# Kernel tuning notes

Hardware: AMD Instinct MI355X
Metric: run time of the kernel (lower is better)

## Reference

```python
import jax, jax.numpy as jnp
import numpy as np

N = 50000      # nodes
E = 1600000    # edges (avg degree 32)
F_IN = 128
HID = 256
C = 40


def setup_inputs() -> dict:
    key = jax.random.key(0)
    ks = jax.random.split(key, 12)
    x = jax.random.normal(ks[0], (N, F_IN), jnp.float32)
    edge_index = jax.random.randint(ks[1], (2, E), 0, N, dtype=jnp.int32)

    def glorot(k, fan_in, fan_out):
        s = jnp.sqrt(2.0 / (fan_in + fan_out)).astype(jnp.float32)
        return jax.random.normal(k, (fan_in, fan_out), jnp.float32) * s

    return {
        "x": x,
        "edge_index": edge_index,
        "W1": glorot(ks[2], F_IN, HID), "b1": jnp.zeros((HID,), jnp.float32),
        "W2": glorot(ks[3], HID, HID),  "b2": jnp.zeros((HID,), jnp.float32),
        "W3": glorot(ks[4], HID, HID),  "b3": jnp.zeros((HID,), jnp.float32),
        "W4": glorot(ks[5], HID, C),    "b4": jnp.zeros((C,), jnp.float32),
    }


def _gcn_conv(x, W, b, src, dst, norm_e, self_norm):
    # PyG GCNConv: h = X W; out_j = sum_i norm_ij * h_i  (+ self-loop term) + b
    h = x @ W                                   # [N, F_out]
    msg = h[src] * norm_e[:, None]              # [E, F_out] gather + scale
    agg = jax.ops.segment_sum(msg, dst, num_segments=N)
    agg = agg + h * self_norm[:, None]          # self-loop contribution
    return agg + b


def reference(x, edge_index, W1, b1, W2, b2, W3, b3, W4, b4):
    src, dst = edge_index[0], edge_index[1]
    # degree on A + I (self-loops added), computed over destination nodes
    deg = jax.ops.segment_sum(jnp.ones((E,), x.dtype), dst, num_segments=N) + 1.0
    inv_sqrt = jax.lax.rsqrt(deg)               # [N]
    norm_e = inv_sqrt[src] * inv_sqrt[dst]      # [E] symmetric norm per edge
    self_norm = inv_sqrt * inv_sqrt             # [N] self-loop norm = 1/deg

    h = jax.nn.relu(_gcn_conv(x, W1, b1, src, dst, norm_e, self_norm))
    h = jax.nn.relu(_gcn_conv(h, W2, b2, src, dst, norm_e, self_norm))
    h = jax.nn.relu(_gcn_conv(h, W3, b3, src, dst, norm_e, self_norm))
    h = _gcn_conv(h, W4, b4, src, dst, norm_e, self_norm)
    return jax.nn.log_softmax(h, axis=1)
```

## Files before the change

### kernel.cpp

```cpp
#include <hip/hip_runtime.h>
#include <hip/hip_fp16.h>
#include <math.h>


typedef _Float16 f16x8 __attribute__((ext_vector_type(8)));
typedef float f32x4 __attribute__((ext_vector_type(4)));

#define CAP 80

#define AS1 __attribute__((address_space(1)))
#define AS3 __attribute__((address_space(3)))

__device__ __forceinline__ void dma16(const unsigned short* g,
                                      const unsigned short* ldsBase) {
    __builtin_amdgcn_global_load_lds((const AS1 void*)(size_t)g,
                                     (AS3 void*)(unsigned)(size_t)ldsBase,
                                     16, 0, 0);
}

__device__ __forceinline__ __half2 u2h2(unsigned u) {
    union { unsigned u; __half2 h; } v; v.u = u; return v.h;
}
__device__ __forceinline__ unsigned h22u(__half2 h) {
    union { unsigned u; __half2 h; } v; v.h = h; return v.u;
}
__device__ __forceinline__ float hlo(unsigned u) {
    return __half2float(__ushort_as_half((unsigned short)(u & 0xFFFFu)));
}
__device__ __forceinline__ float hhi(unsigned u) {
    return __half2float(__ushort_as_half((unsigned short)(u >> 16)));
}

__global__ __launch_bounds__(256) void countprep_kernel(
        const int* __restrict__ src, const int* __restrict__ dst,
        int* __restrict__ cnt, int* __restrict__ rank, int E, int nEdgeBlocks,
        const float* __restrict__ x, unsigned short* __restrict__ xb, int nx4,
        const float* __restrict__ W1, const float* __restrict__ W2,
        const float* __restrict__ W3, const float* __restrict__ W4,
        unsigned short* __restrict__ Wt1, unsigned short* __restrict__ Wt2,
        unsigned short* __restrict__ Wt3, unsigned short* __restrict__ Wt4) {
    int b = blockIdx.x;
    if (b < nEdgeBlocks) {
        int e = b * 256 + threadIdx.x;
        if (e < E) rank[e] = atomicAdd(&cnt[dst[e]], 1);
        return;
    }
    int i = (b - nEdgeBlocks) * 256 + threadIdx.x;
    if (i < nx4) {
        float4 v = reinterpret_cast<const float4*>(x)[i];
        ushort4 o;
        o.x = __half_as_ushort(__float2half_rn(v.x));
        o.y = __half_as_ushort(__float2half_rn(v.y));
        o.z = __half_as_ushort(__float2half_rn(v.z));
        o.w = __half_as_ushort(__float2half_rn(v.w));
        reinterpret_cast<ushort4*>(xb)[i] = o;
        return;
    }
    int j = i - nx4;
    if (j < 32768) {
        int k = j >> 8, n = j & 255;
        Wt1[n * 128 + k] = __half_as_ushort(__float2half_rn(W1[j]));
    } else if (j < 98304) {
        int t = j - 32768; int k = t >> 8, n = t & 255;
        Wt2[n * 256 + k] = __half_as_ushort(__float2half_rn(W2[t]));
    } else if (j < 163840) {
        int t = j - 98304; int k = t >> 8, n = t & 255;
        Wt3[n * 256 + k] = __half_as_ushort(__float2half_rn(W3[t]));
    } else if (j < 174080) {
        int t = j - 163840; int k = t / 40, n = t - k * 40;
        Wt4[n * 256 + k] = __half_as_ushort(__float2half_rn(W4[t]));
    }
}

__global__ __launch_bounds__(256) void rsq_kernel(const int* __restrict__ cnt,
                                                  float* __restrict__ rsq, int N) {
    int n = blockIdx.x * 256 + threadIdx.x;
    if (n < N) rsq[n] = rsqrtf((float)cnt[n] + 1.0f);
}

__global__ __launch_bounds__(256) void scatter_kernel(const int* __restrict__ src,
                                                      const int* __restrict__ dst,
                                                      const int* __restrict__ rank,
                                                      const float* __restrict__ rsq,
                                                      unsigned* __restrict__ epk, int E) {
    int e = blockIdx.x * 256 + threadIdx.x;
    if (e < E) {
        int d = dst[e];
        int s = src[e];
        int r = rank[e]; if (r >= CAP) r = CAP - 1;
        float w = rsq[s] * rsq[d];
        epk[(size_t)d * CAP + r] = (unsigned)s |
                   ((unsigned)__half_as_ushort(__float2half_rn(w)) << 16);
    }
}

template <int H2, bool BIAS, bool RELU>
__global__ __launch_bounds__(256) void agg_f16_kernel(
        const unsigned* __restrict__ G,
        const int* __restrict__ cnt,
        const unsigned* __restrict__ epk,
        const float* __restrict__ rsq,
        const float* __restrict__ bias,
        unsigned* __restrict__ out, int N) {
    constexpr int ROWU = 64 * H2;
    constexpr int UNR = 8;
    int lane = threadIdx.x & 63;
    int node = blockIdx.x * 4 + (threadIdx.x >> 6);
    if (node >= N) return;
    const unsigned* base = G + lane * H2;
    const unsigned* ep = epk + (size_t)node * CAP;
    int deg = cnt[node];

    __half2 acc[H2];
    #pragma unroll
    for (int i = 0; i < H2; i++) acc[i] = u2h2(0u);

    int e = 0;
    for (; e + UNR - 1 < deg; e += UNR) {
        unsigned p[UNR];
        int s[UNR];
        #pragma unroll
        for (int j = 0; j < UNR; j++) { p[j] = ep[e + j]; s[j] = p[j] & 0xFFFFu; }
        unsigned g[UNR][H2];
        #pragma unroll
        for (int j = 0; j < UNR; j++)
            #pragma unroll
            for (int i = 0; i < H2; i++)
                g[j][i] = base[(size_t)s[j] * ROWU + i];
        #pragma unroll
        for (int j = 0; j < UNR; j++) {
            __half2 w2 = __half2half2(__ushort_as_half((unsigned short)(p[j] >> 16)));
            #pragma unroll
            for (int i = 0; i < H2; i++)
                acc[i] = __hfma2(w2, u2h2(g[j][i]), acc[i]);
        }
    }
    for (; e < deg; e++) {
        unsigned p0 = ep[e];
        int s0 = p0 & 0xFFFFu;
        __half2 w2 = __half2half2(__ushort_as_half((unsigned short)(p0 >> 16)));
        #pragma unroll
        for (int i = 0; i < H2; i++)
            acc[i] = __hfma2(w2, u2h2(base[(size_t)s0 * ROWU + i]), acc[i]);
    }

    float sn = rsq[node];
    sn *= sn;
    #pragma unroll
    for (int i = 0; i < H2; i++) {
        unsigned sv = base[(size_t)node * ROWU + i];
        float2 f = __half22float2(acc[i]);
        f.x = fmaf(sn, hlo(sv), f.x);
        f.y = fmaf(sn, hhi(sv), f.y);
        if (BIAS) {
            float2 b = reinterpret_cast<const float2*>(bias)[lane * H2 + i];
            f.x += b.x; f.y += b.y;
        }
        if (RELU) { f.x = fmaxf(f.x, 0.f); f.y = fmaxf(f.y, 0.f); }
        out[(size_t)node * ROWU + lane * H2 + i] = h22u(__floats2half2_rn(f.x, f.y));
    }
}

__global__ __launch_bounds__(256) void agg40_softmax_kernel(
        const unsigned* __restrict__ G,
        const int* __restrict__ cnt,
        const unsigned* __restrict__ epk,
        const float* __restrict__ rsq,
        const float* __restrict__ bias,
        float* __restrict__ out, int N) {
    int lane = threadIdx.x & 63;
    int node = blockIdx.x * 4 + (threadIdx.x >> 6);
    if (node >= N) return;
    bool act = lane < 20;
    int cl = act ? lane : 0;
    const unsigned* ep = epk + (size_t)node * CAP;
    int deg = cnt[node];
    __half2 acch = u2h2(0u);
    int e = 0;
    for (; e + 3 < deg; e += 4) {
        unsigned p[4];
        int s[4];
        #pragma unroll
        for (int j = 0; j < 4; j++) { p[j] = ep[e + j]; s[j] = p[j] & 0xFFFFu; }
        unsigned g[4];
        #pragma unroll
        for (int j = 0; j < 4; j++) g[j] = G[(size_t)s[j] * 20 + cl];
        #pragma unroll
        for (int j = 0; j < 4; j++) {
            __half2 w = __half2half2(__ushort_as_half((unsigned short)(p[j] >> 16)));
            acch = __hfma2(w, u2h2(g[j]), acch);
        }
    }
    for (; e < deg; e++) {
        unsigned p0 = ep[e];
        int s0 = p0 & 0xFFFFu;
        __half2 w0 = __half2half2(__ushort_as_half((unsigned short)(p0 >> 16)));
        acch = __hfma2(w0, u2h2(G[(size_t)s0 * 20 + cl]), acch);
    }
    float lo = 0.f, hi = 0.f;
    if (act) {
        float sn = rsq[node];
        sn *= sn;
        unsigned sv = G[(size_t)node * 20 + lane];
        float2 f = __half22float2(acch);
        lo = fmaf(sn, hlo(sv), f.x) + bias[2 * lane];
        hi = fmaf(sn, hhi(sv), f.y) + bias[2 * lane + 1];
    }
    float m = act ? fmaxf(lo, hi) : -INFINITY;
    #pragma unroll
    for (int o = 32; o >= 1; o >>= 1) m = fmaxf(m, __shfl_xor(m, o, 64));
    float s = act ? (expf(lo - m) + expf(hi - m)) : 0.f;
    #pragma unroll
    for (int o = 32; o >= 1; o >>= 1) s += __shfl_xor(s, o, 64);
    float ls = logf(s);
    if (act) {
        float2 o2;
        o2.x = lo - m - ls;
        o2.y = hi - m - ls;
        *reinterpret_cast<float2*>(out + (size_t)node * 40 + 2 * lane) = o2;
    }
}

template <bool BIAS, bool RELU>
__global__ __launch_bounds__(256) void gemm_f16(
        const unsigned short* __restrict__ A,
        const unsigned short* __restrict__ Bt,
        const float* __restrict__ bias,
        unsigned short* __restrict__ Cout,
        int M, int K, int Nc) {
    __shared__ __align__(16) unsigned short As[128 * 64];
    __shared__ __align__(16) unsigned short Bs[128 * 64];
    int tid = threadIdx.x;
    int lane = tid & 63;
    int wid = tid >> 6;
    int rowBase = blockIdx.y * 128;
    int colBase = blockIdx.x * 128;
    int waveM = (wid & 1) * 64;
    int waveN = (wid >> 1) * 64;

    f32x4 acc[4][4] = {};
    int lrow = lane & 15;
    int kgrp = (lane >> 4) * 8;

    for (int k0 = 0; k0 < K; k0 += 64) {
        #pragma unroll
        for (int c = 0; c < 4; c++) {
            int base16 = c * 256 + wid * 64;
            int slot = base16 + lane;
            int row = slot >> 3;
            int kp = (slot & 7) * 8;
            int ksw = kp ^ ((row & 7) * 8);
            int gr = rowBase + row; if (gr >= M) gr = M - 1;
            dma16(A + (size_t)gr * K + k0 + ksw, &As[base16 * 8]);
            int gc = colBase + row; if (gc >= Nc) gc = Nc - 1;
            dma16(Bt + (size_t)gc * K + k0 + ksw, &Bs[base16 * 8]);
        }
        __syncthreads();
        #pragma unroll
        for (int kk = 0; kk < 64; kk += 32) {
            f16x8 af[4], bfr[4];
            #pragma unroll
            for (int t = 0; t < 4; t++) {
                int ra = waveM + t * 16 + lrow;
                af[t] = *reinterpret_cast<const f16x8*>(
                    &As[ra * 64 + ((kk + kgrp) ^ ((ra & 7) * 8))]);
                int rb = waveN + t * 16 + lrow;
                bfr[t] = *reinterpret_cast<const f16x8*>(
                    &Bs[rb * 64 + ((kk + kgrp) ^ ((rb & 7) * 8))]);
            }
            #pragma unroll
            for (int mt = 0; mt < 4; mt++)
                #pragma unroll
                for (int nt = 0; nt < 4; nt++)
                    acc[mt][nt] = __builtin_amdgcn_mfma_f32_16x16x32_f16(
                        af[mt], bfr[nt], acc[mt][nt], 0, 0, 0);
        }
        __syncthreads();
    }

    #pragma unroll
    for (int mt = 0; mt < 4; mt++) {
        #pragma unroll
        for (int r = 0; r < 4; r++) {
            int row = rowBase + waveM + mt * 16 + (lane >> 4) * 4 + r;
            if (row >= M) continue;
            #pragma unroll
            for (int nt = 0; nt < 4; nt++) {
                int col = colBase + waveN + nt * 16 + (lane & 15);
                if (col >= Nc) continue;
                float v = acc[mt][nt][r];
                if (BIAS) v += bias[col];
                if (RELU) v = fmaxf(v, 0.f);
                Cout[(size_t)row * Nc + col] = __half_as_ushort(__float2half_rn(v));
            }
        }
    }
}


extern "C" void kernel_launch(void* const* d_in, const int* in_sizes, int n_in,
                              void* d_out, int out_size, void* d_ws, size_t ws_size,
                              hipStream_t stream) {
    const float* x  = (const float*)d_in[0];
    const int*   ei = (const int*)d_in[1];
    const float* W1 = (const float*)d_in[2];
    const float* b1 = (const float*)d_in[3];
    const float* W2 = (const float*)d_in[4];
    const float* b2 = (const float*)d_in[5];
    const float* W3 = (const float*)d_in[6];
    const float* b3 = (const float*)d_in[7];
    const float* W4 = (const float*)d_in[8];
    const float* b4 = (const float*)d_in[9];

    const int FIN = 128, HID = 256, C = 40;
    const int N = in_sizes[0] / FIN;
    const int E = in_sizes[1] / 2;
    const int* src = ei;
    const int* dst = ei + E;

    char* w = (char*)d_ws;
    auto alloc = [&](size_t bytes) {
        char* p = w;
        w += (bytes + 255) & ~(size_t)255;
        return p;
    };
    int*   cnt    = (int*)alloc((size_t)N * 4);
    float* rsq    = (float*)alloc((size_t)N * 4);
    unsigned* epk = (unsigned*)alloc((size_t)N * CAP * 4);
    unsigned short* aggx = (unsigned short*)alloc((size_t)N * FIN * 2);
    unsigned short* bufA = (unsigned short*)alloc((size_t)N * HID * 2);
    unsigned short* bufB = (unsigned short*)alloc((size_t)N * HID * 2);
    unsigned short* Wt1 = (unsigned short*)alloc((size_t)FIN * HID * 2);
    unsigned short* Wt2 = (unsigned short*)alloc((size_t)HID * HID * 2);
    unsigned short* Wt3 = (unsigned short*)alloc((size_t)HID * HID * 2);
    unsigned short* Wt4 = (unsigned short*)alloc((size_t)HID * C * 2);
    int* rank = (int*)aggx;
    unsigned short* xb = bufB;

    hipMemsetAsync(cnt, 0, (size_t)N * 4, stream);

    int nx4 = N * FIN / 4;
    int nEdgeBlocks = (E + 255) / 256;
    int prepBlocks = (nx4 + 174080 + 255) / 256;
    countprep_kernel<<<nEdgeBlocks + prepBlocks, 256, 0, stream>>>(
        src, dst, cnt, rank, E, nEdgeBlocks,
        x, xb, nx4, W1, W2, W3, W4, Wt1, Wt2, Wt3, Wt4);
    rsq_kernel<<<(N + 255) / 256, 256, 0, stream>>>(cnt, rsq, N);
    scatter_kernel<<<nEdgeBlocks, 256, 0, stream>>>(src, dst, rank, rsq, epk, E);

    int grp = (N + 3) / 4;
    dim3 gHID((HID + 127) / 128, (N + 127) / 128);
    dim3 gC((C + 127) / 128, (N + 127) / 128);

    agg_f16_kernel<1, false, false>
        <<<grp, 256, 0, stream>>>((const unsigned*)xb, cnt, epk, rsq, nullptr,
                                  (unsigned*)aggx, N);
    gemm_f16<true, true><<<gHID, 256, 0, stream>>>(aggx, Wt1, b1, bufA, N, FIN, HID);
    gemm_f16<false, false><<<gHID, 256, 0, stream>>>(bufA, Wt2, nullptr, bufB,
                                                     N, HID, HID);
    agg_f16_kernel<2, true, true>
        <<<grp, 256, 0, stream>>>((const unsigned*)bufB, cnt, epk, rsq, b2,
                                  (unsigned*)bufA, N);
    gemm_f16<false, false><<<gHID, 256, 0, stream>>>(bufA, Wt3, nullptr, bufB,
                                                     N, HID, HID);
    agg_f16_kernel<2, true, true>
        <<<grp, 256, 0, stream>>>((const unsigned*)bufB, cnt, epk, rsq, b3,
                                  (unsigned*)bufA, N);
    gemm_f16<false, false><<<gC, 256, 0, stream>>>(bufA, Wt4, nullptr, bufB,
                                                   N, HID, C);
    agg40_softmax_kernel<<<grp, 256, 0, stream>>>((const unsigned*)bufB, cnt, epk,
                                                  rsq, b4, (float*)d_out, N);
}
```

Before: 585.4 us.

## Fold symmetric norm into node-side scaling and shrink edge lists to 16-bit indices

The separate scatter kernel goes away: the count kernel now writes 16-bit source indices straight into the capped per-node adjacency slots. Per-edge weights are no longer stored. The D^-1/2 factors are moved onto node rows instead: hidden features are kept pre-scaled by rsq, so later aggregations become plain half-precision adds, and the output scaling, bias and ReLU are applied per node in the epilogue. The GEMM K-tile is also raised to 128. This cuts edge-list bandwidth in half and drops one kernel launch, at the cost of extra rsq gathers in the first layer and different fp16 rounding behaviour.

```diff
diff --git a/kernel.cpp b/kernel.cpp
--- a/kernel.cpp
+++ b/kernel.cpp
@@ -31,9 +31,10 @@
     return __half2float(__ushort_as_half((unsigned short)(u >> 16)));
 }
 
-__global__ __launch_bounds__(256) void countprep_kernel(
+__global__ __launch_bounds__(256) void build_prep_kernel(
         const int* __restrict__ src, const int* __restrict__ dst,
-        int* __restrict__ cnt, int* __restrict__ rank, int E, int nEdgeBlocks,
+        int* __restrict__ cnt, unsigned short* __restrict__ epk,
+        int E, int nEdgeBlocks,
         const float* __restrict__ x, unsigned short* __restrict__ xb, int nx4,
         const float* __restrict__ W1, const float* __restrict__ W2,
         const float* __restrict__ W3, const float* __restrict__ W4,
@@ -42,7 +43,12 @@
     int b = blockIdx.x;
     if (b < nEdgeBlocks) {
         int e = b * 256 + threadIdx.x;
-        if (e < E) rank[e] = atomicAdd(&cnt[dst[e]], 1);
+        if (e < E) {
+            int d = dst[e];
+            int s = src[e];
+            int r = atomicAdd(&cnt[d], 1);
+            if (r < CAP) epk[(size_t)d * CAP + r] = (unsigned short)s;
+        }
         return;
     }
     int i = (b - nEdgeBlocks) * 256 + threadIdx.x;
@@ -78,93 +84,101 @@
     if (n < N) rsq[n] = rsqrtf((float)cnt[n] + 1.0f);
 }
 
-__global__ __launch_bounds__(256) void scatter_kernel(const int* __restrict__ src,
-                                                      const int* __restrict__ dst,
-                                                      const int* __restrict__ rank,
-                                                      const float* __restrict__ rsq,
-                                                      unsigned* __restrict__ epk, int E) {
-    int e = blockIdx.x * 256 + threadIdx.x;
-    if (e < E) {
-        int d = dst[e];
-        int s = src[e];
-        int r = rank[e]; if (r >= CAP) r = CAP - 1;
-        float w = rsq[s] * rsq[d];
-        epk[(size_t)d * CAP + r] = (unsigned)s |
-                   ((unsigned)__half_as_ushort(__float2half_rn(w)) << 16);
-    }
-}
-
-template <int H2, bool BIAS, bool RELU>
-__global__ __launch_bounds__(256) void agg_f16_kernel(
+template <int H2, bool WSRC, bool BIAS, bool RELU>
+__global__ __launch_bounds__(256) void agg_sum_kernel(
         const unsigned* __restrict__ G,
         const int* __restrict__ cnt,
-        const unsigned* __restrict__ epk,
+        const unsigned short* __restrict__ epk,
         const float* __restrict__ rsq,
         const float* __restrict__ bias,
         unsigned* __restrict__ out, int N) {
     constexpr int ROWU = 64 * H2;
-    constexpr int UNR = 8;
     int lane = threadIdx.x & 63;
     int node = blockIdx.x * 4 + (threadIdx.x >> 6);
     if (node >= N) return;
     const unsigned* base = G + lane * H2;
-    const unsigned* ep = epk + (size_t)node * CAP;
-    int deg = cnt[node];
+    const unsigned short* ep = epk + (size_t)node * CAP;
+    int deg = cnt[node]; if (deg > CAP) deg = CAP;
 
     __half2 acc[H2];
     #pragma unroll
     for (int i = 0; i < H2; i++) acc[i] = u2h2(0u);
 
     int e = 0;
-    for (; e + UNR - 1 < deg; e += UNR) {
-        unsigned p[UNR];
-        int s[UNR];
-        #pragma unroll
-        for (int j = 0; j < UNR; j++) { p[j] = ep[e + j]; s[j] = p[j] & 0xFFFFu; }
-        unsigned g[UNR][H2];
-        #pragma unroll
-        for (int j = 0; j < UNR; j++)
+    for (; e + 7 < deg; e += 8) {
+        uint4 pv = *reinterpret_cast<const uint4*>(ep + e);
+        int s[8];
+        s[0] = pv.x & 0xFFFFu; s[1] = pv.x >> 16;
+        s[2] = pv.y & 0xFFFFu; s[3] = pv.y >> 16;
+        s[4] = pv.z & 0xFFFFu; s[5] = pv.z >> 16;
+        s[6] = pv.w & 0xFFFFu; s[7] = pv.w >> 16;
+        float ws[8];
+        if (WSRC) {
+            #pragma unroll
+            for (int j = 0; j < 8; j++) ws[j] = rsq[s[j]];
+        }
+        unsigned g[8][H2];
+        #pragma unroll
+        for (int j = 0; j < 8; j++)
             #pragma unroll
             for (int i = 0; i < H2; i++)
                 g[j][i] = base[(size_t)s[j] * ROWU + i];
         #pragma unroll
-        for (int j = 0; j < UNR; j++) {
-            __half2 w2 = __half2half2(__ushort_as_half((unsigned short)(p[j] >> 16)));
+        for (int j = 0; j < 8; j++) {
+            if (WSRC) {
+                __half2 w2 = __half2half2(__float2half_rn(ws[j]));
+                #pragma unroll
+                for (int i = 0; i < H2; i++)
+                    acc[i] = __hfma2(w2, u2h2(g[j][i]), acc[i]);
+            } else {
+                #pragma unroll
+                for (int i = 0; i < H2; i++)
+                    acc[i] = __hadd2(acc[i], u2h2(g[j][i]));
+            }
+        }
+    }
+    for (; e < deg; e++) {
+        int s0 = ep[e];
+        if (WSRC) {
+            __half2 w2 = __half2half2(__float2half_rn(rsq[s0]));
             #pragma unroll
             for (int i = 0; i < H2; i++)
-                acc[i] = __hfma2(w2, u2h2(g[j][i]), acc[i]);
-        }
-    }
-    for (; e < deg; e++) {
-        unsigned p0 = ep[e];
-        int s0 = p0 & 0xFFFFu;
-        __half2 w2 = __half2half2(__ushort_as_half((unsigned short)(p0 >> 16)));
-        #pragma unroll
-        for (int i = 0; i < H2; i++)
-            acc[i] = __hfma2(w2, u2h2(base[(size_t)s0 * ROWU + i]), acc[i]);
-    }
-
-    float sn = rsq[node];
-    sn *= sn;
+                acc[i] = __hfma2(w2, u2h2(base[(size_t)s0 * ROWU + i]), acc[i]);
+        } else {
+            #pragma unroll
+            for (int i = 0; i < H2; i++)
+                acc[i] = __hadd2(acc[i], u2h2(base[(size_t)s0 * ROWU + i]));
+        }
+    }
+
+    float r = rsq[node];
+    float sw = WSRC ? r : 1.0f;
     #pragma unroll
     for (int i = 0; i < H2; i++) {
+        float2 f = __half22float2(acc[i]);
         unsigned sv = base[(size_t)node * ROWU + i];
-        float2 f = __half22float2(acc[i]);
-        f.x = fmaf(sn, hlo(sv), f.x);
-        f.y = fmaf(sn, hhi(sv), f.y);
-        if (BIAS) {
-            float2 b = reinterpret_cast<const float2*>(bias)[lane * H2 + i];
-            f.x += b.x; f.y += b.y;
-        }
-        if (RELU) { f.x = fmaxf(f.x, 0.f); f.y = fmaxf(f.y, 0.f); }
-        out[(size_t)node * ROWU + lane * H2 + i] = h22u(__floats2half2_rn(f.x, f.y));
+        f.x = fmaf(sw, hlo(sv), f.x);
+        f.y = fmaf(sw, hhi(sv), f.y);
+        float ox, oy;
+        if (WSRC) {
+            ox = r * f.x; oy = r * f.y;
+        } else {
+            float r2 = r * r;
+            ox = r2 * f.x; oy = r2 * f.y;
+            if (BIAS) {
+                float2 bv = reinterpret_cast<const float2*>(bias)[lane * H2 + i];
+                ox = fmaf(r, bv.x, ox); oy = fmaf(r, bv.y, oy);
+            }
+            if (RELU) { ox = fmaxf(ox, 0.f); oy = fmaxf(oy, 0.f); }
+        }
+        out[(size_t)node * ROWU + lane * H2 + i] = h22u(__floats2half2_rn(ox, oy));
     }
 }
 
 __global__ __launch_bounds__(256) void agg40_softmax_kernel(
         const unsigned* __restrict__ G,
         const int* __restrict__ cnt,
-        const unsigned* __restrict__ epk,
+        const unsigned short* __restrict__ epk,
         const float* __restrict__ rsq,
         const float* __restrict__ bias,
         float* __restrict__ out, int N) {
@@ -173,38 +187,35 @@
     if (node >= N) return;
     bool act = lane < 20;
     int cl = act ? lane : 0;
-    const unsigned* ep = epk + (size_t)node * CAP;
-    int deg = cnt[node];
+    const unsigned short* ep = epk + (size_t)node * CAP;
+    int deg = cnt[node]; if (deg > CAP) deg = CAP;
     __half2 acch = u2h2(0u);
     int e = 0;
-    for (; e + 3 < deg; e += 4) {
-        unsigned p[4];
-        int s[4];
-        #pragma unroll
-        for (int j = 0; j < 4; j++) { p[j] = ep[e + j]; s[j] = p[j] & 0xFFFFu; }
-        unsigned g[4];
-        #pragma unroll
-        for (int j = 0; j < 4; j++) g[j] = G[(size_t)s[j] * 20 + cl];
-        #pragma unroll
-        for (int j = 0; j < 4; j++) {
-            __half2 w = __half2half2(__ushort_as_half((unsigned short)(p[j] >> 16)));
-            acch = __hfma2(w, u2h2(g[j]), acch);
-        }
+    for (; e + 7 < deg; e += 8) {
+        uint4 pv = *reinterpret_cast<const uint4*>(ep + e);
+        int s[8];
+        s[0] = pv.x & 0xFFFFu; s[1] = pv.x >> 16;
+        s[2] = pv.y & 0xFFFFu; s[3] = pv.y >> 16;
+        s[4] = pv.z & 0xFFFFu; s[5] = pv.z >> 16;
+        s[6] = pv.w & 0xFFFFu; s[7] = pv.w >> 16;
+        unsigned g[8];
+        #pragma unroll
+        for (int j = 0; j < 8; j++) g[j] = G[(size_t)s[j] * 20 + cl];
+        #pragma unroll
+        for (int j = 0; j < 8; j++) acch = __hadd2(acch, u2h2(g[j]));
     }
     for (; e < deg; e++) {
-        unsigned p0 = ep[e];
-        int s0 = p0 & 0xFFFFu;
-        __half2 w0 = __half2half2(__ushort_as_half((unsigned short)(p0 >> 16)));
-        acch = __hfma2(w0, u2h2(G[(size_t)s0 * 20 + cl]), acch);
+        int s0 = ep[e];
+        acch = __hadd2(acch, u2h2(G[(size_t)s0 * 20 + cl]));
     }
     float lo = 0.f, hi = 0.f;
     if (act) {
-        float sn = rsq[node];
-        sn *= sn;
+        float r = rsq[node];
         unsigned sv = G[(size_t)node * 20 + lane];
         float2 f = __half22float2(acch);
-        lo = fmaf(sn, hlo(sv), f.x) + bias[2 * lane];
-        hi = fmaf(sn, hhi(sv), f.y) + bias[2 * lane + 1];
+        f.x += hlo(sv); f.y += hhi(sv);
+        lo = fmaf(r, f.x, bias[2 * lane]);
+        hi = fmaf(r, f.y, bias[2 * lane + 1]);
     }
     float m = act ? fmaxf(lo, hi) : -INFINITY;
     #pragma unroll
@@ -221,15 +232,18 @@
     }
 }
 
-template <bool BIAS, bool RELU>
+template <int BK, bool BIAS, bool RELU, bool SCALE>
 __global__ __launch_bounds__(256) void gemm_f16(
         const unsigned short* __restrict__ A,
         const unsigned short* __restrict__ Bt,
         const float* __restrict__ bias,
+        const float* __restrict__ rsqRow,
         unsigned short* __restrict__ Cout,
         int M, int K, int Nc) {
-    __shared__ __align__(16) unsigned short As[128 * 64];
-    __shared__ __align__(16) unsigned short Bs[128 * 64];
+    constexpr int SPR = BK / 8;
+    constexpr int NSTG = (128 * SPR) / 256;
+    __shared__ __align__(16) unsigned short As[128 * BK];
+    __shared__ __align__(16) unsigned short Bs[128 * BK];
     int tid = threadIdx.x;
     int lane = tid & 63;
     int wid = tid >> 6;
@@ -242,14 +256,14 @@
     int lrow = lane & 15;
     int kgrp = (lane >> 4) * 8;
 
-    for (int k0 = 0; k0 < K; k0 += 64) {
-        #pragma unroll
-        for (int c = 0; c < 4; c++) {
+    for (int k0 = 0; k0 < K; k0 += BK) {
+        #pragma unroll
+        for (int c = 0; c < NSTG; c++) {
             int base16 = c * 256 + wid * 64;
             int slot = base16 + lane;
-            int row = slot >> 3;
-            int kp = (slot & 7) * 8;
-            int ksw = kp ^ ((row & 7) * 8);
+            int row = slot / SPR;
+            int kp = (slot % SPR) * 8;
+            int ksw = kp ^ ((row & (SPR - 1)) * 8);
             int gr = rowBase + row; if (gr >= M) gr = M - 1;
             dma16(A + (size_t)gr * K + k0 + ksw, &As[base16 * 8]);
             int gc = colBase + row; if (gc >= Nc) gc = Nc - 1;
@@ -257,16 +271,16 @@
         }
         __syncthreads();
         #pragma unroll
-        for (int kk = 0; kk < 64; kk += 32) {
+        for (int kk = 0; kk < BK; kk += 32) {
             f16x8 af[4], bfr[4];
             #pragma unroll
             for (int t = 0; t < 4; t++) {
                 int ra = waveM + t * 16 + lrow;
                 af[t] = *reinterpret_cast<const f16x8*>(
-                    &As[ra * 64 + ((kk + kgrp) ^ ((ra & 7) * 8))]);
+                    &As[ra * BK + ((kk + kgrp) ^ ((ra & (SPR - 1)) * 8))]);
                 int rb = waveN + t * 16 + lrow;
                 bfr[t] = *reinterpret_cast<const f16x8*>(
-                    &Bs[rb * 64 + ((kk + kgrp) ^ ((rb & 7) * 8))]);
+                    &Bs[rb * BK + ((kk + kgrp) ^ ((rb & (SPR - 1)) * 8))]);
             }
             #pragma unroll
             for (int mt = 0; mt < 4; mt++)
@@ -284,6 +298,7 @@
         for (int r = 0; r < 4; r++) {
             int row = rowBase + waveM + mt * 16 + (lane >> 4) * 4 + r;
             if (row >= M) continue;
+            float rs = SCALE ? rsqRow[row] : 1.0f;
             #pragma unroll
             for (int nt = 0; nt < 4; nt++) {
                 int col = colBase + waveN + nt * 16 + (lane & 15);
@@ -291,6 +306,7 @@
                 float v = acc[mt][nt][r];
                 if (BIAS) v += bias[col];
                 if (RELU) v = fmaxf(v, 0.f);
+                if (SCALE) v *= rs;
                 Cout[(size_t)row * Nc + col] = __half_as_ushort(__float2half_rn(v));
             }
         }
@@ -326,7 +342,7 @@
     };
     int*   cnt    = (int*)alloc((size_t)N * 4);
     float* rsq    = (float*)alloc((size_t)N * 4);
-    unsigned* epk = (unsigned*)alloc((size_t)N * CAP * 4);
+    unsigned short* epk = (unsigned short*)alloc((size_t)N * CAP * 2);
     unsigned short* aggx = (unsigned short*)alloc((size_t)N * FIN * 2);
     unsigned short* bufA = (unsigned short*)alloc((size_t)N * HID * 2);
     unsigned short* bufB = (unsigned short*)alloc((size_t)N * HID * 2);
@@ -334,7 +350,6 @@
     unsigned short* Wt2 = (unsigned short*)alloc((size_t)HID * HID * 2);
     unsigned short* Wt3 = (unsigned short*)alloc((size_t)HID * HID * 2);
     unsigned short* Wt4 = (unsigned short*)alloc((size_t)HID * C * 2);
-    int* rank = (int*)aggx;
     unsigned short* xb = bufB;
 
     hipMemsetAsync(cnt, 0, (size_t)N * 4, stream);
@@ -342,32 +357,32 @@
     int nx4 = N * FIN / 4;
     int nEdgeBlocks = (E + 255) / 256;
     int prepBlocks = (nx4 + 174080 + 255) / 256;
-    countprep_kernel<<<nEdgeBlocks + prepBlocks, 256, 0, stream>>>(
-        src, dst, cnt, rank, E, nEdgeBlocks,
+    build_prep_kernel<<<nEdgeBlocks + prepBlocks, 256, 0, stream>>>(
+        src, dst, cnt, epk, E, nEdgeBlocks,
         x, xb, nx4, W1, W2, W3, W4, Wt1, Wt2, Wt3, Wt4);
     rsq_kernel<<<(N + 255) / 256, 256, 0, stream>>>(cnt, rsq, N);
-    scatter_kernel<<<nEdgeBlocks, 256, 0, stream>>>(src, dst, rank, rsq, epk, E);
 
     int grp = (N + 3) / 4;
     dim3 gHID((HID + 127) / 128, (N + 127) / 128);
     dim3 gC((C + 127) / 128, (N + 127) / 128);
 
-    agg_f16_kernel<1, false, false>
+    agg_sum_kernel<1, true, false, false>
         <<<grp, 256, 0, stream>>>((const unsigned*)xb, cnt, epk, rsq, nullptr,
                                   (unsigned*)aggx, N);
-    gemm_f16<true, true><<<gHID, 256, 0, stream>>>(aggx, Wt1, b1, bufA, N, FIN, HID);
-    gemm_f16<false, false><<<gHID, 256, 0, stream>>>(bufA, Wt2, nullptr, bufB,
-                                                     N, HID, HID);
-    agg_f16_kernel<2, true, true>
+    gemm_f16<128, true, true, true><<<gHID, 256, 0, stream>>>(
+        aggx, Wt1, b1, rsq, bufA, N, FIN, HID);
+    gemm_f16<128, false, false, false><<<gHID, 256, 0, stream>>>(
+        bufA, Wt2, nullptr, nullptr, bufB, N, HID, HID);
+    agg_sum_kernel<2, false, true, true>
         <<<grp, 256, 0, stream>>>((const unsigned*)bufB, cnt, epk, rsq, b2,
                                   (unsigned*)bufA, N);
-    gemm_f16<false, false><<<gHID, 256, 0, stream>>>(bufA, Wt3, nullptr, bufB,
-                                                     N, HID, HID);
-    agg_f16_kernel<2, true, true>
+    gemm_f16<128, false, false, false><<<gHID, 256, 0, stream>>>(
+        bufA, Wt3, nullptr, nullptr, bufB, N, HID, HID);
+    agg_sum_kernel<2, false, true, true>
         <<<grp, 256, 0, stream>>>((const unsigned*)bufB, cnt, epk, rsq, b3,
                                   (unsigned*)bufA, N);
-    gemm_f16<false, false><<<gC, 256, 0, stream>>>(bufA, Wt4, nullptr, bufB,
-                                                   N, HID, C);
+    gemm_f16<128, false, false, false><<<gC, 256, 0, stream>>>(
+        bufA, Wt4, nullptr, nullptr, bufB, N, HID, C);
     agg40_softmax_kernel<<<grp, 256, 0, stream>>>((const unsigned*)bufB, cnt, epk,
                                                   rsq, b4, (float*)d_out, N);
 }
```

Measured after the change: 621.9 us. +6.2%, slower.
